# Performance work log

Hardware: AMD Instinct MI355X
Metric: run time of the kernel (lower is better)

Reference implementation:

```python
import jax, jax.numpy as jnp
import numpy as np

M_RANGE = 3
K = 2 * M_RANGE + 1          # kernel size = 7
N_CLASS = K * K              # 49 motion classes
IM_CHANNEL = 3


def setup_inputs() -> dict:
    key = jax.random.key(0)
    k1, k2, k3, k4 = jax.random.split(key, 4)
    B, H, W = 16, 256, 256
    im_input = jax.random.normal(k1, (B, 2 * IM_CHANNEL, H, W), dtype=jnp.float32)
    im_output = jax.random.normal(k2, (B, IM_CHANNEL, H, W), dtype=jnp.float32)
    # motion in [-M_RANGE, M_RANGE-1) so that floor(m)+M_RANGE+1 <= K-1 (valid bin)
    gt_motion = jax.random.uniform(k3, (B, 2, H, W), dtype=jnp.float32) * (2 * M_RANGE - 1) - M_RANGE
    # grouped-conv weight (already in post-swapaxes [n_class, 1, K, K] layout)
    m_kernel = jax.random.uniform(k4, (N_CLASS, 1, K, K), dtype=jnp.float32)
    return {"im_input": im_input, "im_output": im_output,
            "gt_motion": gt_motion, "m_kernel": m_kernel}


def _axis_weights(m):
    # m: [B,H,W] -> bilinear binning weights over K bins: [B,H,W,K]
    f = jnp.floor(m)
    frac = m - f
    idx = f.astype(jnp.int32) + M_RANGE
    oh0 = jax.nn.one_hot(idx, K, dtype=m.dtype)
    oh1 = jax.nn.one_hot(idx + 1, K, dtype=m.dtype)
    return (1.0 - frac)[..., None] * oh0 + frac[..., None] * oh1


def motion2mask(motion):
    # faithful vectorization of the triple-loop: mask[c=iy*K+ix] = b[iy]*a[ix]
    ax = _axis_weights(motion[:, 0])   # x-motion -> columns of ger(b, a)
    ay = _axis_weights(motion[:, 1])   # y-motion -> rows
    mask = ay[..., :, None] * ax[..., None, :]       # [B,H,W,K,K] outer product
    B, H, W = motion.shape[0], motion.shape[2], motion.shape[3]
    return mask.reshape(B, H, W, N_CLASS).transpose(0, 3, 1, 2)  # [B,N_CLASS,H,W]


def _conv(x, w, groups):
    return jax.lax.conv_general_dilated(
        x, w, window_strides=(1, 1),
        padding=[(M_RANGE, M_RANGE), (M_RANGE, M_RANGE)],
        dimension_numbers=("NCHW", "OIHW", "NCHW"),
        feature_group_count=groups)


def reference(im_input, im_output, gt_motion, m_kernel):
    m_mask = motion2mask(gt_motion)                   # [B,N_CLASS,H,W]
    out_mask = _conv(m_mask, m_kernel, N_CLASS)       # grouped conv, same shape
    im = im_input[:, -IM_CHANNEL:]                    # [B,3,H,W]
    B, C, H, W = im.shape
    # construct_image: each channel expanded to N_CLASS copies then grouped-conv
    # == plain conv of each single channel with all N_CLASS kernels
    nearby = _conv(im.reshape(B * C, 1, H, W), m_kernel, 1)
    nearby = nearby.reshape(B, C, N_CLASS, H, W)
    pred = (nearby * out_mask[:, None]).sum(axis=2)   # [B,3,H,W]
    return pred, m_mask
```

## Files before the change

### kernel.cpp

```cpp
#include <hip/hip_runtime.h>

typedef __bf16 bf16x8 __attribute__((ext_vector_type(8)));
typedef float  f32x4  __attribute__((ext_vector_type(4)));

#define TILE   16
#define HALO   22
#define KK     7
#define NCLASS 49
#define IMW    256
#define IMH    256
#define HW     65536
#define HH     484
#define OMS    57
#define KPW    56

__device__ __forceinline__ unsigned pack2bf(float a, float b) {
    unsigned ua = __float_as_uint(a);
    unsigned ub = __float_as_uint(b);
    ua = (ua + 0x7fffu + ((ua >> 16) & 1u)) >> 16;
    ub = (ub + 0x7fffu + ((ub >> 16) & 1u)) & 0xffff0000u;
    return (ua & 0xffffu) | ub;
}

__global__ __launch_bounds__(256, 2)
void gtnet_kernel(const float* __restrict__ im_input,
                  const float* __restrict__ gt_motion,
                  const float* __restrict__ m_kernel,
                  float* __restrict__ out_pred,
                  float* __restrict__ out_mask)
{
    __shared__ float omW[256 * OMS];
    __shared__ unsigned KP2[NCLASS * KPW];
    __shared__ float2 halo[HH];
    __shared__ __align__(16) float iml4[HH * 4];

    const int tid  = threadIdx.x;
    const int lane = tid & 63, wv_id = tid >> 6;
    const int tx = tid & 15, ty = tid >> 4;
    const int x0 = blockIdx.x * TILE, y0 = blockIdx.y * TILE;
    const int b  = blockIdx.z;
    const int x = x0 + tx, y = y0 + ty;

    for (int i = tid; i < NCLASS * KPW; i += 256) {
        int s = i / KPW, n = i - s * KPW;
        float a  = (n < NCLASS)     ? m_kernel[n * NCLASS + s]       : 0.0f;
        float b2 = (n + 1 < NCLASS) ? m_kernel[(n + 1) * NCLASS + s] : 0.0f;
        KP2[i] = pack2bf(a, b2);
    }

    const float* mot_x = gt_motion + (size_t)b * 2 * HW;
    const float* mot_y = mot_x + HW;
    for (int i = tid; i < HH; i += 256) {
        int hy = i / HALO, hx = i - hy * HALO;
        int gy = y0 - 3 + hy, gx = x0 - 3 + hx;
        float2 v;
        if (gy >= 0 && gy < IMH && gx >= 0 && gx < IMW) {
            int off = gy * IMW + gx;
            v.x = mot_y[off] + 3.0f;
            v.y = mot_x[off] + 3.0f;
        } else {
            v.x = -8.0f; v.y = -8.0f;
        }
        halo[i] = v;
    }

    const float* imP = im_input + ((size_t)b * 6 + 3) * HW;
    for (int i = tid; i < HH; i += 256) {
        int hy = i / HALO, hx = i - hy * HALO;
        int gy = y0 - 3 + hy, gx = x0 - 3 + hx;
        float4 v = {0.0f, 0.0f, 0.0f, 0.0f};
        if (gy >= 0 && gy < IMH && gx >= 0 && gx < IMW) {
            int off = gy * IMW + gx;
            v.x = imP[off];
            v.y = imP[off + HW];
            v.z = imP[off + 2 * HW];
        }
        *reinterpret_cast<float4*>(&iml4[i * 4]) = v;
    }

    {
        float2* omv = reinterpret_cast<float2*>(omW);
        for (int i = tid; i < 256 * OMS / 2; i += 256) omv[i] = make_float2(0.0f, 0.0f);
    }

    __syncthreads();

    {
        float2 h = halo[(ty + 3) * HALO + (tx + 3)];
        float iyf = floorf(h.x), ixf = floorf(h.y);
        float fy = h.x - iyf,    fx = h.y - ixf;
        int   iy = (int)iyf,     ix = (int)ixf;
        float wyA[KK], wxB[KK];
        #pragma unroll
        for (int a = 0; a < KK; a++) {
            wyA[a] = (a == iy) ? (1.0f - fy) : ((a == iy + 1) ? fy : 0.0f);
            wxB[a] = (a == ix) ? (1.0f - fx) : ((a == ix + 1) ? fx : 0.0f);
        }
        float* mm = out_mask + (size_t)b * NCLASS * HW + y * IMW + x;
        #pragma unroll
        for (int a = 0; a < KK; a++)
            #pragma unroll
            for (int bb = 0; bb < KK; bb++)
                mm[(size_t)(a * KK + bb) * HW] = wyA[a] * wxB[bb];
    }

    float* const omRow = &omW[tid * OMS];
    #pragma unroll
    for (int u = 0; u < KK; u++) {
        #pragma unroll
        for (int v = 0; v < KK; v++) {
            const int s = u * KK + v;
            float2 h = halo[(ty + u) * HALO + (tx + v)];
            float ayc = h.x, axc = h.y;
            float iyf = floorf(ayc), ixf = floorf(axc);
            float fy = ayc - iyf,    fx = axc - ixf;
            bool  valid = (ayc >= 0.0f);
            float wy0 = valid ? (1.0f - fy) : 0.0f;
            float wy1 = valid ? fy : 0.0f;
            int   n00 = valid ? ((int)iyf * KK + (int)ixf) : 0;
            unsigned pA = KP2[s * KPW + n00];
            unsigned pB = KP2[s * KPW + n00 + KK];
            float k00 = __uint_as_float(pA << 16);
            float k01 = __uint_as_float(pA & 0xffff0000u);
            float k10 = __uint_as_float(pB << 16);
            float k11 = __uint_as_float(pB & 0xffff0000u);
            float wx0 = 1.0f - fx;
            float* ob = omRow + n00;
            float o0 = ob[0], o1 = ob[1];
            float o7 = ob[KK], o8 = ob[KK + 1];
            ob[0]      = fmaf(wy0 * wx0, k00, o0);
            ob[1]      = fmaf(wy0 * fx , k01, o1);
            ob[KK]     = fmaf(wy1 * wx0, k10, o7);
            ob[KK + 1] = fmaf(wy1 * fx , k11, o8);
        }
    }

    __syncthreads();

    bf16x8 af[2][4];
    #pragma unroll
    for (int kit = 0; kit < 2; kit++) {
        #pragma unroll
        for (int mt = 0; mt < 4; mt++) {
            int px  = wv_id * 64 + mt * 16 + (lane & 15);
            int k0  = kit * 32 + (lane >> 4) * 8;
            int k0r = (k0 > 48) ? 49 : k0;
            const float* r = &omW[px * OMS + k0r];
            bf16x8 a;
            #pragma unroll
            for (int j = 0; j < 8; j++) a[j] = (__bf16)r[j];
            af[kit][mt] = a;
        }
    }
    bf16x8 bfr[2][4];
    #pragma unroll
    for (int kit = 0; kit < 2; kit++) {
        #pragma unroll
        for (int nt = 0; nt < 4; nt++) {
            int t   = nt * 16 + (lane & 15);
            int k0  = kit * 32 + (lane >> 4) * 8;
            int k0r = (k0 > 48) ? 49 : k0;
            union { unsigned u[4]; bf16x8 v; } bu;
            #pragma unroll
            for (int j = 0; j < 4; j++) bu.u[j] = KP2[t * KPW + k0r + 2 * j];
            bfr[kit][nt] = bu.v;
        }
    }

    __syncthreads();

    f32x4 acc[4][4];
    #pragma unroll
    for (int mt = 0; mt < 4; mt++) {
        #pragma unroll
        for (int nt = 0; nt < 4; nt++) {
            f32x4 c = {0.0f, 0.0f, 0.0f, 0.0f};
            c = __builtin_amdgcn_mfma_f32_16x16x32_bf16(af[0][mt], bfr[0][nt], c, 0, 0, 0);
            c = __builtin_amdgcn_mfma_f32_16x16x32_bf16(af[1][mt], bfr[1][nt], c, 0, 0, 0);
            acc[mt][nt] = c;
        }
    }

    #pragma unroll
    for (int mt = 0; mt < 4; mt++) {
        #pragma unroll
        for (int nt = 0; nt < 4; nt++) {
            int t = nt * 16 + (lane & 15);
            if (t < NCLASS) {
                #pragma unroll
                for (int r = 0; r < 4; r++) {
                    int px = wv_id * 64 + mt * 16 + (lane >> 4) * 4 + r;
                    omW[px * OMS + t] = acc[mt][nt][r];
                }
            }
        }
    }

    __syncthreads();

    float wv[NCLASS];
    #pragma unroll
    for (int t = 0; t < NCLASS; t++) wv[t] = omW[tid * OMS + t];

    float a0 = 0.0f, a1 = 0.0f, a2 = 0.0f;
    #pragma unroll
    for (int p = 0; p < KK; p++) {
        #pragma unroll
        for (int q = 0; q < KK; q++) {
            float wvv = wv[p * KK + q];
            int   hi = (ty + p) * HALO + (tx + q);
            float4 im3 = *reinterpret_cast<const float4*>(&iml4[hi * 4]);
            a0 = fmaf(wvv, im3.x, a0);
            a1 = fmaf(wvv, im3.y, a1);
            a2 = fmaf(wvv, im3.z, a2);
        }
    }
    float* pr = out_pred + (size_t)b * 3 * HW + y * IMW + x;
    pr[0]      = a0;
    pr[HW]     = a1;
    pr[2 * HW] = a2;
}

extern "C" void kernel_launch(void* const* d_in, const int* in_sizes, int n_in,
                              void* d_out, int out_size, void* d_ws, size_t ws_size,
                              hipStream_t stream) {
    const float* im_input  = (const float*)d_in[0];
    const float* gt_motion = (const float*)d_in[2];
    const float* m_kernel  = (const float*)d_in[3];

    float* pred = (float*)d_out;
    float* mask = pred + (size_t)16 * 3 * HW;

    dim3 grid(IMW / TILE, IMH / TILE, 16);
    dim3 block(256);
    hipLaunchKernelGGL(gtnet_kernel, grid, block, 0, stream,
                       im_input, gt_motion, m_kernel, pred, mask);
}
```

Baseline: 379.5 us.

## Precompute per-pixel motion weights in halo and scatter packed fp16 pairs

The halo stage now precomputes the bilinear weights as packed half2 values and the row indices, so the 49-tap scatter loop skips repeated floor and index math. The per-pixel accumulator is reorganised into even/odd-paired half2 rows laid out column-major by thread, which should reduce LDS bank conflicts and halve the read-modify-write traffic. MFMA switches from bf16 to fp16, with A fragments rebuilt from the even/odd rows. The mask stage reads motion straight from global memory. Accumulating in fp16 gives lower precision than the previous fp32 accumulator.

```diff
diff --git a/kernel.cpp b/kernel.cpp
--- a/kernel.cpp
+++ b/kernel.cpp
@@ -1,7 +1,8 @@
 #include <hip/hip_runtime.h>
-
-typedef __bf16 bf16x8 __attribute__((ext_vector_type(8)));
-typedef float  f32x4  __attribute__((ext_vector_type(4)));
+#include <hip/hip_fp16.h>
+
+typedef _Float16 f16x8 __attribute__((ext_vector_type(8)));
+typedef float    f32x4 __attribute__((ext_vector_type(4)));
 
 #define TILE   16
 #define HALO   22
@@ -11,16 +12,11 @@
 #define IMH    256
 #define HW     65536
 #define HH     484
-#define OMS    57
-#define KPW    56
-
-__device__ __forceinline__ unsigned pack2bf(float a, float b) {
-    unsigned ua = __float_as_uint(a);
-    unsigned ub = __float_as_uint(b);
-    ua = (ua + 0x7fffu + ((ua >> 16) & 1u)) >> 16;
-    ub = (ub + 0x7fffu + ((ub >> 16) & 1u)) & 0xffff0000u;
-    return (ua & 0xffffu) | ub;
-}
+#define WST    52
+
+__device__ __forceinline__ unsigned h2u(__half2 h) { union { __half2 h; unsigned u; } c; c.h = h; return c.u; }
+__device__ __forceinline__ __half2  u2h(unsigned u) { union { __half2 h; unsigned u; } c; c.u = u; return c.h; }
+__device__ __forceinline__ int rowOf(int n) { return (n & 1) ? (25 + (n >> 1)) : (n >> 1); }
 
 __global__ __launch_bounds__(256, 2)
 void gtnet_kernel(const float* __restrict__ im_input,
@@ -29,9 +25,9 @@
                   float* __restrict__ out_pred,
                   float* __restrict__ out_mask)
 {
-    __shared__ float omW[256 * OMS];
-    __shared__ unsigned KP2[NCLASS * KPW];
-    __shared__ float2 halo[HH];
+    __shared__ __align__(16) unsigned omP[256 * WST];
+    __shared__ unsigned KB[NCLASS * NCLASS];
+    __shared__ uint4    haloP[HH];
     __shared__ __align__(16) float iml4[HH * 4];
 
     const int tid  = threadIdx.x;
@@ -41,11 +37,13 @@
     const int b  = blockIdx.z;
     const int x = x0 + tx, y = y0 + ty;
 
-    for (int i = tid; i < NCLASS * KPW; i += 256) {
-        int s = i / KPW, n = i - s * KPW;
-        float a  = (n < NCLASS)     ? m_kernel[n * NCLASS + s]       : 0.0f;
-        float b2 = (n + 1 < NCLASS) ? m_kernel[(n + 1) * NCLASS + s] : 0.0f;
-        KP2[i] = pack2bf(a, b2);
+    for (int i = tid; i < NCLASS * NCLASS; i += 256) {
+        int s = i / NCLASS, r = i - s * NCLASS;
+        int n0 = (r < 25) ? (2 * r) : (2 * (r - 25) + 1);
+        int n1 = n0 + 1;
+        float k0 = m_kernel[n0 * NCLASS + s];
+        float k1 = (n1 < NCLASS) ? m_kernel[n1 * NCLASS + s] : 0.f;
+        KB[i] = h2u(__halves2half2(__float2half_rn(k0), __float2half_rn(k1)));
     }
 
     const float* mot_x = gt_motion + (size_t)b * 2 * HW;
@@ -53,15 +51,22 @@
     for (int i = tid; i < HH; i += 256) {
         int hy = i / HALO, hx = i - hy * HALO;
         int gy = y0 - 3 + hy, gx = x0 - 3 + hx;
-        float2 v;
+        uint4 e;
         if (gy >= 0 && gy < IMH && gx >= 0 && gx < IMW) {
             int off = gy * IMW + gx;
-            v.x = mot_y[off] + 3.0f;
-            v.y = mot_x[off] + 3.0f;
+            float ay = mot_y[off] + 3.0f;
+            float ax = mot_x[off] + 3.0f;
+            float iyf = floorf(ay), ixf = floorf(ax);
+            float fy = ay - iyf,    fx = ax - ixf;
+            int   n00 = (int)iyf * KK + (int)ixf;
+            e.x = h2u(__halves2half2(__float2half_rn(1.0f - fy), __float2half_rn(fy)));
+            e.y = h2u(__halves2half2(__float2half_rn(1.0f - fx), __float2half_rn(fx)));
+            e.z = (unsigned)((rowOf(n00) << 16) | rowOf(n00 + KK));
+            e.w = 0;
         } else {
-            v.x = -8.0f; v.y = -8.0f;
-        }
-        halo[i] = v;
+            e.x = 0; e.y = 0; e.z = (0u << 16) | 28u; e.w = 0;
+        }
+        haloP[i] = e;
     }
 
     const float* imP = im_input + ((size_t)b * 6 + 3) * HW;
@@ -79,24 +84,27 @@
     }
 
     {
-        float2* omv = reinterpret_cast<float2*>(omW);
-        for (int i = tid; i < 256 * OMS / 2; i += 256) omv[i] = make_float2(0.0f, 0.0f);
+        uint4* p = reinterpret_cast<uint4*>(omP);
+        for (int i = tid; i < (NCLASS * 256) / 4 + 1; i += 256)
+            if (i * 4 < NCLASS * 256 + 4) p[i] = make_uint4(0, 0, 0, 0);
     }
 
     __syncthreads();
 
     {
-        float2 h = halo[(ty + 3) * HALO + (tx + 3)];
-        float iyf = floorf(h.x), ixf = floorf(h.y);
-        float fy = h.x - iyf,    fx = h.y - ixf;
-        int   iy = (int)iyf,     ix = (int)ixf;
+        int off = y * IMW + x;
+        float ay = mot_y[off] + 3.0f;
+        float ax = mot_x[off] + 3.0f;
+        float iyf = floorf(ay), ixf = floorf(ax);
+        float fy = ay - iyf,    fx = ax - ixf;
+        int   iy = (int)iyf,    ix = (int)ixf;
         float wyA[KK], wxB[KK];
         #pragma unroll
         for (int a = 0; a < KK; a++) {
             wyA[a] = (a == iy) ? (1.0f - fy) : ((a == iy + 1) ? fy : 0.0f);
             wxB[a] = (a == ix) ? (1.0f - fx) : ((a == ix + 1) ? fx : 0.0f);
         }
-        float* mm = out_mask + (size_t)b * NCLASS * HW + y * IMW + x;
+        float* mm = out_mask + (size_t)b * NCLASS * HW + off;
         #pragma unroll
         for (int a = 0; a < KK; a++)
             #pragma unroll
@@ -104,65 +112,75 @@
                 mm[(size_t)(a * KK + bb) * HW] = wyA[a] * wxB[bb];
     }
 
-    float* const omRow = &omW[tid * OMS];
     #pragma unroll
     for (int u = 0; u < KK; u++) {
         #pragma unroll
         for (int v = 0; v < KK; v++) {
             const int s = u * KK + v;
-            float2 h = halo[(ty + u) * HALO + (tx + v)];
-            float ayc = h.x, axc = h.y;
-            float iyf = floorf(ayc), ixf = floorf(axc);
-            float fy = ayc - iyf,    fx = axc - ixf;
-            bool  valid = (ayc >= 0.0f);
-            float wy0 = valid ? (1.0f - fy) : 0.0f;
-            float wy1 = valid ? fy : 0.0f;
-            int   n00 = valid ? ((int)iyf * KK + (int)ixf) : 0;
-            unsigned pA = KP2[s * KPW + n00];
-            unsigned pB = KP2[s * KPW + n00 + KK];
-            float k00 = __uint_as_float(pA << 16);
-            float k01 = __uint_as_float(pA & 0xffff0000u);
-            float k10 = __uint_as_float(pB << 16);
-            float k11 = __uint_as_float(pB & 0xffff0000u);
-            float wx0 = 1.0f - fx;
-            float* ob = omRow + n00;
-            float o0 = ob[0], o1 = ob[1];
-            float o7 = ob[KK], o8 = ob[KK + 1];
-            ob[0]      = fmaf(wy0 * wx0, k00, o0);
-            ob[1]      = fmaf(wy0 * fx , k01, o1);
-            ob[KK]     = fmaf(wy1 * wx0, k10, o7);
-            ob[KK + 1] = fmaf(wy1 * fx , k11, o8);
-        }
-    }
-
-    __syncthreads();
-
-    bf16x8 af[2][4];
+            uint4 hp = haloP[(ty + u) * HALO + (tx + v)];
+            __half2 wy = u2h(hp.x);
+            __half2 wx = u2h(hp.y);
+            int rowA = (int)(hp.z >> 16), rowB = (int)(hp.z & 0xffffu);
+            __half2 kA = u2h(KB[s * NCLASS + rowA]);
+            __half2 kB = u2h(KB[s * NCLASS + rowB]);
+            __half2 cA = __hmul2(__hmul2(__low2half2(wy),  wx), kA);
+            __half2 cB = __hmul2(__hmul2(__high2half2(wy), wx), kB);
+            unsigned* pA = &omP[rowA * 256 + tid];
+            unsigned* pB = &omP[rowB * 256 + tid];
+            *pA = h2u(__hadd2(u2h(*pA), cA));
+            *pB = h2u(__hadd2(u2h(*pB), cB));
+        }
+    }
+
+    __syncthreads();
+
+    f16x8 af[2][4];
     #pragma unroll
     for (int kit = 0; kit < 2; kit++) {
         #pragma unroll
         for (int mt = 0; mt < 4; mt++) {
+            int kk0 = kit * 32 + (lane >> 4) * 8;
+            int rE  = kk0 >> 1;
             int px  = wv_id * 64 + mt * 16 + (lane & 15);
-            int k0  = kit * 32 + (lane >> 4) * 8;
-            int k0r = (k0 > 48) ? 49 : k0;
-            const float* r = &omW[px * OMS + k0r];
-            bf16x8 a;
-            #pragma unroll
-            for (int j = 0; j < 8; j++) a[j] = (__bf16)r[j];
-            af[kit][mt] = a;
-        }
-    }
-    bf16x8 bfr[2][4];
+            unsigned Ew[4], Ow[5];
+            #pragma unroll
+            for (int i2 = 0; i2 < 4; i2++) {
+                int r = rE + i2;
+                unsigned val = omP[r * 256 + px];
+                Ew[i2] = (r <= 24) ? val : 0u;
+            }
+            #pragma unroll
+            for (int j = 0; j < 5; j++) {
+                int o   = rE - 1 + j;
+                int row = 25 + o;
+                row = (row > 48) ? 48 : row;
+                unsigned val = omP[row * 256 + px];
+                Ow[j] = (o >= 0 && o <= 23) ? val : 0u;
+            }
+            union { unsigned u[4]; f16x8 v; } au;
+            #pragma unroll
+            for (int i2 = 0; i2 < 4; i2++) {
+                unsigned oal = (Ow[i2 + 1] << 16) | (Ow[i2] >> 16);
+                au.u[i2] = h2u(__hadd2(u2h(Ew[i2]), u2h(oal)));
+            }
+            af[kit][mt] = au.v;
+        }
+    }
+    f16x8 bfr[2][4];
     #pragma unroll
     for (int kit = 0; kit < 2; kit++) {
         #pragma unroll
         for (int nt = 0; nt < 4; nt++) {
             int t   = nt * 16 + (lane & 15);
-            int k0  = kit * 32 + (lane >> 4) * 8;
-            int k0r = (k0 > 48) ? 49 : k0;
-            union { unsigned u[4]; bf16x8 v; } bu;
-            #pragma unroll
-            for (int j = 0; j < 4; j++) bu.u[j] = KP2[t * KPW + k0r + 2 * j];
+            int kk0 = kit * 32 + (lane >> 4) * 8;
+            int rE  = kk0 >> 1;
+            union { unsigned u[4]; f16x8 v; } bu;
+            #pragma unroll
+            for (int j = 0; j < 4; j++) {
+                int r = rE + j;
+                unsigned val = KB[t * NCLASS + r];
+                bu.u[j] = (r <= 24) ? val : 0u;
+            }
             bfr[kit][nt] = bu.v;
         }
     }
@@ -175,12 +193,13 @@
         #pragma unroll
         for (int nt = 0; nt < 4; nt++) {
             f32x4 c = {0.0f, 0.0f, 0.0f, 0.0f};
-            c = __builtin_amdgcn_mfma_f32_16x16x32_bf16(af[0][mt], bfr[0][nt], c, 0, 0, 0);
-            c = __builtin_amdgcn_mfma_f32_16x16x32_bf16(af[1][mt], bfr[1][nt], c, 0, 0, 0);
+            c = __builtin_amdgcn_mfma_f32_16x16x32_f16(af[0][mt], bfr[0][nt], c, 0, 0, 0);
+            c = __builtin_amdgcn_mfma_f32_16x16x32_f16(af[1][mt], bfr[1][nt], c, 0, 0, 0);
             acc[mt][nt] = c;
         }
     }
 
+    float* Wf = reinterpret_cast<float*>(omP);
     #pragma unroll
     for (int mt = 0; mt < 4; mt++) {
         #pragma unroll
@@ -190,7 +209,7 @@
                 #pragma unroll
                 for (int r = 0; r < 4; r++) {
                     int px = wv_id * 64 + mt * 16 + (lane >> 4) * 4 + r;
-                    omW[px * OMS + t] = acc[mt][nt][r];
+                    Wf[px * WST + t] = acc[mt][nt][r];
                 }
             }
         }
@@ -200,7 +219,7 @@
 
     float wv[NCLASS];
     #pragma unroll
-    for (int t = 0; t < NCLASS; t++) wv[t] = omW[tid * OMS + t];
+    for (int t = 0; t < NCLASS; t++) wv[t] = Wf[tid * WST + t];
 
     float a0 = 0.0f, a1 = 0.0f, a2 = 0.0f;
     #pragma unroll
```

New measurement: 356.7 us. -6.0%, faster.
